# Optimization experiments

Measured on AMD Instinct MI355X. Metric: run time of the kernel, lower is better.

The kernel has to match this reference:

```python
import jax, jax.numpy as jnp
import numpy as np

N, E, G = 50000, 1600000, 500
H, F, NG, L, OUT = 128, 128, 50, 6, 1
LOG2 = float(np.log(2.0))

def ssp(x):
    return jax.nn.softplus(x) - LOG2

def setup_inputs() -> dict:
    key = jax.random.key(0)
    ks = jax.random.split(key, 16)
    inp = {
        'z': jax.random.randint(ks[0], (N,), 0, 100),
        'pos': jax.random.normal(ks[1], (N, 3), jnp.float32) * 5.0,
        'batch': jnp.sort(jax.random.randint(ks[2], (N,), 0, G)),
        'edge_index': jax.random.randint(ks[3], (2, E), 0, N),
        # parameters
        'emb': jax.random.normal(ks[4], (100, H), jnp.float32) * 0.1,
        'dist_W': jax.random.normal(ks[5], (1, NG), jnp.float32) * 0.1,
        'dist_b': jnp.zeros((NG,), jnp.float32),
        'Wn': jax.random.normal(ks[6], (L, H, F), jnp.float32) * (1.0 / np.sqrt(H)),
        'We': jax.random.normal(ks[7], (L, NG, F), jnp.float32) * (1.0 / np.sqrt(NG)),
        'be': jnp.zeros((L, F), jnp.float32),
        'Wo': jax.random.normal(ks[8], (L, F, H), jnp.float32) * (1.0 / np.sqrt(F)),
        'bo': jnp.zeros((L, H), jnp.float32),
        'W1': jax.random.normal(ks[9], (H, H // 2), jnp.float32) * (1.0 / np.sqrt(H)),
        'b1': jnp.zeros((H // 2,), jnp.float32),
        'W2': jax.random.normal(ks[10], (H // 2, OUT), jnp.float32) * (1.0 / np.sqrt(H // 2)),
        'b2': jnp.zeros((OUT,), jnp.float32),
    }
    return inp

def reference(z, pos, batch, edge_index, emb, dist_W, dist_b, Wn, We, be, Wo, bo, W1, b1, W2, b2):
    row, col = edge_index[0], edge_index[1]
    # edge distances -> Linear(1, num_gaussians)
    dist = jnp.linalg.norm(pos[row] - pos[col], axis=-1)            # [E]
    e = dist[:, None] * dist_W[0][None, :] + dist_b                 # [E, NG]
    v = emb[z]                                                      # [N, H]
    # edge-conditioned message passing x num_layers
    for i in range(Wn.shape[0]):
        h = v @ Wn[i]                                               # [N, F]
        msg = h[col] * (e @ We[i] + be[i])                          # [E, F]
        agg = jax.ops.segment_sum(msg, row, num_segments=v.shape[0])
        v = ssp(agg @ Wo[i] + bo[i])                                # [N, H]
    # readout
    u = ssp(v @ W1 + b1) @ W2 + b2                                  # [N, OUT]
    return jax.ops.segment_sum(u, batch, num_segments=G)            # [G, OUT]
```

## Files before the change

kernel.cpp:

```cpp
#include <hip/hip_runtime.h>
#include <math.h>

#define HDIM 128
#define NGAUSS 50
#define NLAYER 6
#define TSTR 136
#define DINV (1.0f/512.0f)
#define NXCD 8
#define NSTRIPE 512

typedef unsigned short ushortT;
typedef __attribute__((ext_vector_type(8))) short bf16x8;
typedef __attribute__((ext_vector_type(4))) float f32x4;

static __device__ __forceinline__ float bf2f(unsigned short u){
  union { unsigned int i; float f; } x; x.i = ((unsigned int)u) << 16; return x.f;
}
static __device__ __forceinline__ float bitsf(unsigned int i){
  union { unsigned int i; float f; } x; x.i = i; return x.f;
}
static __device__ __forceinline__ unsigned short f2bf(float f){
  union { float f; unsigned int i; } x; x.f = f;
  unsigned int i = x.i;
  unsigned int r = (i + 0x7FFFu + ((i >> 16) & 1u)) >> 16;
  return (unsigned short)r;
}
static __device__ __forceinline__ float ssp(float x){
  return fmaxf(x, 0.0f) + __logf(1.0f + __expf(-fabsf(x))) - 0.69314718055994530942f;
}
static __device__ __forceinline__ f32x4 mfma4r(const bf16x8* a, const bf16x8* b){
  f32x4 d = {0.f, 0.f, 0.f, 0.f};
  d = __builtin_amdgcn_mfma_f32_16x16x32_bf16(a[0], b[0], d, 0, 0, 0);
  d = __builtin_amdgcn_mfma_f32_16x16x32_bf16(a[1], b[1], d, 0, 0, 0);
  d = __builtin_amdgcn_mfma_f32_16x16x32_bf16(a[2], b[2], d, 0, 0, 0);
  d = __builtin_amdgcn_mfma_f32_16x16x32_bf16(a[3], b[3], d, 0, 0, 0);
  return d;
}


__global__ __launch_bounds__(256)
void k_hist(const int* __restrict__ erow, int* __restrict__ hist,
            int E, int NB, int shift, int estripe){
  __shared__ int lh[512];
  int tid = threadIdx.x, w = blockIdx.x;
  for (int i = tid; i < NB; i += 256) lh[i] = 0;
  __syncthreads();
  int beg = w * estripe;
  int end = beg + estripe; if (end > E) end = E;
  for (int e = beg + tid; e < end; e += 256)
    atomicAdd(&lh[erow[e] >> shift], 1);
  __syncthreads();
  for (int i = tid; i < NB; i += 256) hist[w * 512 + i] = lh[i];
}

__global__ __launch_bounds__(256)
void k_colscan(int* __restrict__ hist, int* __restrict__ colTotal, int NB){
  __shared__ int sA[512], sB[512];
  int b = blockIdx.x, tid = threadIdx.x;
  sA[tid]       = hist[tid * 512 + b];
  sA[tid + 256] = hist[(tid + 256) * 512 + b];
  __syncthreads();
  int* pa = sA; int* pb = sB;
  for (int off = 1; off < 512; off <<= 1){
    for (int i = tid; i < 512; i += 256)
      pb[i] = pa[i] + (i >= off ? pa[i - off] : 0);
    __syncthreads();
    int* t = pa; pa = pb; pb = t;
  }
  int e0 = (tid == 0) ? 0 : pa[tid - 1];
  int e1 = pa[tid + 255];
  hist[tid * 512 + b]       = e0;
  hist[(tid + 256) * 512 + b] = e1;
  if (tid == 0) colTotal[b] = pa[511];
}

__global__ __launch_bounds__(256)
void k_bscan(const int* __restrict__ colTotal, int* __restrict__ bucketBase, int NB){
  __shared__ int sA[512], sB[512];
  int tid = threadIdx.x;
  for (int i = tid; i < 512; i += 256) sA[i] = (i < NB) ? colTotal[i] : 0;
  __syncthreads();
  int* pa = sA; int* pb = sB;
  for (int off = 1; off < 512; off <<= 1){
    for (int i = tid; i < 512; i += 256)
      pb[i] = pa[i] + (i >= off ? pa[i - off] : 0);
    __syncthreads();
    int* t = pa; pa = pb; pb = t;
  }
  for (int i = tid; i < NB; i += 256)
    bucketBase[i] = (i == 0) ? 0 : pa[i - 1];
  if (tid == 0) bucketBase[NB] = pa[NB - 1];
}

__global__ __launch_bounds__(256)
void k_scatter(const int* __restrict__ erow, const int* __restrict__ ecol,
               const float* __restrict__ pos, const int* __restrict__ hist,
               const int* __restrict__ bucketBase, uint2* __restrict__ stg,
               int E, int NB, int shift, int estripe){
  __shared__ int cur[512];
  int tid = threadIdx.x, w = blockIdx.x;
  for (int b = tid; b < NB; b += 256)
    cur[b] = bucketBase[b] + hist[w * 512 + b];
  __syncthreads();
  int beg = w * estripe;
  int end = beg + estripe; if (end > E) end = E;
  int mask = (1 << shift) - 1;
  for (int e = beg + tid; e < end; e += 256){
    int r = erow[e], c = ecol[e];
    float dx = pos[r*3+0] - pos[c*3+0];
    float dy = pos[r*3+1] - pos[c*3+1];
    float dz = pos[r*3+2] - pos[c*3+2];
    float d = sqrtf(dx*dx + dy*dy + dz*dz);
    int du = (int)(d * 512.0f + 0.5f);
    if (du > 65535) du = 65535;
    int p = atomicAdd(&cur[r >> shift], 1);
    uint2 t;
    t.x = ((unsigned int)c << 16) | (unsigned int)du;
    t.y = (unsigned int)(r & mask);
    stg[p] = t;
  }
}

__global__ __launch_bounds__(256)
void k_place(const uint2* __restrict__ stg, const int* __restrict__ bucketBase,
             int* __restrict__ offsets, unsigned int* __restrict__ csr,
             int N, int NB, int shift, int E){
  __shared__ int rc[1024];
  __shared__ int sA[1024], sB[1024];
  int b = blockIdx.x, tid = threadIdx.x;
  int R = 1 << shift;
  int r0 = b << shift;
  int s = bucketBase[b], e2 = bucketBase[b + 1];
  for (int i = tid; i < R; i += 256) rc[i] = 0;
  __syncthreads();
  for (int j = s + tid; j < e2; j += 256)
    atomicAdd(&rc[stg[j].y], 1);
  __syncthreads();
  for (int i = tid; i < R; i += 256) sA[i] = rc[i];
  __syncthreads();
  int* pa = sA; int* pb = sB;
  for (int off = 1; off < R; off <<= 1){
    for (int i = tid; i < R; i += 256)
      pb[i] = pa[i] + (i >= off ? pa[i - off] : 0);
    __syncthreads();
    int* t = pa; pa = pb; pb = t;
  }
  for (int i = tid; i < R; i += 256){
    int excl = (i == 0) ? 0 : pa[i - 1];
    rc[i] = excl;
    int r = r0 + i;
    if (r < N) offsets[r] = s + excl;
  }
  if (b == NB - 1 && tid == 0) offsets[N] = E;
  __syncthreads();
  for (int j = s + tid; j < e2; j += 256){
    uint2 t = stg[j];
    int slot = s + atomicAdd(&rc[t.y], 1);
    csr[slot] = t.x;
  }
}

__global__ void k_setup(const int* __restrict__ z, const float* __restrict__ emb,
                        ushortT* __restrict__ vhi,
                        const float* __restrict__ Wn, ushortT* __restrict__ WnT,
                        const float* __restrict__ Wo, ushortT* __restrict__ WoT,
                        const float* __restrict__ dW, const float* __restrict__ db,
                        const float* __restrict__ We, const float* __restrict__ be,
                        float* __restrict__ a, float* __restrict__ c,
                        const int* __restrict__ batch, int* __restrict__ groupOff,
                        const float* __restrict__ W1, ushortT* __restrict__ W1T,
                        int N, int G, int B1, int B2, int B4, int B5, int B7){
  int b = blockIdx.x;
  int tid = threadIdx.x;
  if (b < B1){
    int idx = b * 256 + tid;
    if (idx < N * HDIM){
      int n = idx >> 7, f = idx & 127;
      vhi[idx] = f2bf(emb[z[n] * HDIM + f]);
    }
    return;
  }
  b -= B1;
  if (b < B2){
    int idx = b * 256 + tid;
    if (idx < NLAYER * HDIM * HDIM){
      int mat = idx >> 14, rem = idx & 16383;
      int n = rem >> 7, k = rem & 127;
      WnT[idx] = f2bf(Wn[(mat << 14) + k * HDIM + n]);
    }
    return;
  }
  b -= B2;
  if (b < B2){
    int idx = b * 256 + tid;
    if (idx < NLAYER * HDIM * HDIM){
      int mat = idx >> 14, rem = idx & 16383;
      int n = rem >> 7, k = rem & 127;
      WoT[idx] = f2bf(Wo[(mat << 14) + k * HDIM + n]);
    }
    return;
  }
  b -= B2;
  if (b < B4){
    int idx = b * 256 + tid;
    if (idx < NLAYER * HDIM){
      int l = idx >> 7, f = idx & 127;
      float av = 0.f, cv = 0.f;
      for (int g = 0; g < NGAUSS; ++g){
        float we = We[(l * NGAUSS + g) * HDIM + f];
        av += dW[g] * we;
        cv += db[g] * we;
      }
      a[idx] = av;
      c[idx] = cv + be[idx];
    }
    return;
  }
  b -= B4;
  if (b < B5){
    int i = b * 256 + tid;
    if (i >= N) return;
    int bb = batch[i];
    if (i == 0){
      for (int g = 0; g <= bb; ++g) groupOff[g] = 0;
    } else {
      int pb = batch[i - 1];
      for (int g = pb + 1; g <= bb; ++g) groupOff[g] = i;
    }
    if (i == N - 1){
      for (int g = bb + 1; g <= G; ++g) groupOff[g] = N;
    }
    return;
  }
  b -= B5;
  if (b < B7){
    int idx = b * 256 + tid;
    if (idx < 64 * HDIM){
      int ncol = idx >> 7, k = idx & 127;
      W1T[idx] = f2bf(W1[k * 64 + ncol]);
    }
  }
}

__global__ __launch_bounds__(128, 2)
void k_gemm0(const ushortT* __restrict__ X, const ushortT* __restrict__ WT,
             ushortT* __restrict__ outHi, int N){
  int tid = threadIdx.x;
  int wave = tid >> 6, lane = tid & 63;
  int m = lane & 15, quad = lane >> 4;
  int ntiles = (N + 15) >> 4;
  int t0 = (blockIdx.x * 2 + wave) * 2;
  if (t0 >= ntiles) return;

  bf16x8 av[2][4];
  #pragma unroll
  for (int rt = 0; rt < 2; ++rt){
    int row = (t0 + rt) * 16 + m; if (row >= N) row = N - 1;
    #pragma unroll
    for (int kk = 0; kk < 4; ++kk)
      av[rt][kk] = *(const bf16x8*)(X + ((size_t)row << 7) + kk*32 + quad*8);
  }
  #pragma unroll
  for (int ct = 0; ct < 8; ++ct){
    int ncol = ct * 16 + m;
    const ushortT* bp = WT + ((size_t)ncol << 7) + quad*8;
    bf16x8 bb[4];
    #pragma unroll
    for (int kk = 0; kk < 4; ++kk) bb[kk] = *(const bf16x8*)(bp + kk*32);
    #pragma unroll
    for (int rt = 0; rt < 2; ++rt){
      f32x4 d = mfma4r(av[rt], bb);
      #pragma unroll
      for (int r = 0; r < 4; ++r){
        int orow = (t0 + rt) * 16 + quad*4 + r;
        if (orow < N) outHi[((size_t)orow << 7) + ncol] = f2bf(d[r]);
      }
    }
  }
}

#define AGG_PROC(P, DD) do { \
    unsigned int w_; float lo_, hi_; \
    w_ = (P).x; lo_ = bitsf(w_ << 16); hi_ = bitsf(w_ & 0xFFFF0000u); \
    s1[0] = fmaf(lo_, (DD), s1[0]); s0[0] += lo_; \
    s1[1] = fmaf(hi_, (DD), s1[1]); s0[1] += hi_; \
    w_ = (P).y; lo_ = bitsf(w_ << 16); hi_ = bitsf(w_ & 0xFFFF0000u); \
    s1[2] = fmaf(lo_, (DD), s1[2]); s0[2] += lo_; \
    s1[3] = fmaf(hi_, (DD), s1[3]); s0[3] += hi_; \
    w_ = (P).z; lo_ = bitsf(w_ << 16); hi_ = bitsf(w_ & 0xFFFF0000u); \
    s1[4] = fmaf(lo_, (DD), s1[4]); s0[4] += lo_; \
    s1[5] = fmaf(hi_, (DD), s1[5]); s0[5] += hi_; \
    w_ = (P).w; lo_ = bitsf(w_ << 16); hi_ = bitsf(w_ & 0xFFFF0000u); \
    s1[6] = fmaf(lo_, (DD), s1[6]); s0[6] += lo_; \
    s1[7] = fmaf(hi_, (DD), s1[7]); s0[7] += hi_; \
  } while(0)

#define GATH(Q) (*(const uint4*)(h + ((size_t)((Q) >> 16) << 7) + fl))

__global__ __launch_bounds__(256, 6)
void k_agg2(const ushortT* __restrict__ h, const int* __restrict__ offsets,
            const unsigned int* __restrict__ cd, const float* __restrict__ a,
            const float* __restrict__ c, ushortT* __restrict__ aggHi,
            int N, int segNodes){
  int xcd = blockIdx.x & (NXCD - 1);
  int idx = blockIdx.x >> 3;
  int node = xcd * segNodes + idx * 4 + (threadIdx.x >> 6);
  if (node >= N || node >= (xcd + 1) * segNodes) return;
  int lane = threadIdx.x & 63;
  int quarter = lane >> 4;
  int fl = (lane & 15) * 8;
  int s = offsets[node], e = offsets[node + 1];
  float s0[8] = {0.f,0.f,0.f,0.f,0.f,0.f,0.f,0.f};
  float s1[8] = {0.f,0.f,0.f,0.f,0.f,0.f,0.f,0.f};
  int efull = s + ((e - s) & ~7);
  int L = s;
  if (efull - s >= 16){
    unsigned int qA0 = cd[L + quarter],      qA1 = cd[L + 4 + quarter];
    uint4 pA0 = GATH(qA0), pA1 = GATH(qA1);
    unsigned int qB0 = cd[L + 8 + quarter],  qB1 = cd[L + 12 + quarter];
    uint4 pB0 = GATH(qB0), pB1 = GATH(qB1);
    float dA0 = (float)(qA0 & 0xFFFFu) * DINV, dA1 = (float)(qA1 & 0xFFFFu) * DINV;
    float dB0 = (float)(qB0 & 0xFFFFu) * DINV, dB1 = (float)(qB1 & 0xFFFFu) * DINV;
    L += 16;
    for (; L + 16 <= efull; L += 16){
      unsigned int nA0 = cd[L + quarter], nA1 = cd[L + 4 + quarter];
      AGG_PROC(pA0, dA0); AGG_PROC(pA1, dA1);
      pA0 = GATH(nA0); pA1 = GATH(nA1);
      dA0 = (float)(nA0 & 0xFFFFu) * DINV; dA1 = (float)(nA1 & 0xFFFFu) * DINV;
      unsigned int nB0 = cd[L + 8 + quarter], nB1 = cd[L + 12 + quarter];
      AGG_PROC(pB0, dB0); AGG_PROC(pB1, dB1);
      pB0 = GATH(nB0); pB1 = GATH(nB1);
      dB0 = (float)(nB0 & 0xFFFFu) * DINV; dB1 = (float)(nB1 & 0xFFFFu) * DINV;
    }
    AGG_PROC(pA0, dA0); AGG_PROC(pA1, dA1);
    AGG_PROC(pB0, dB0); AGG_PROC(pB1, dB1);
  }
  for (; L + 8 <= efull; L += 8){
    unsigned int q0 = cd[L + quarter], q1 = cd[L + 4 + quarter];
    uint4 p0 = GATH(q0), p1 = GATH(q1);
    float d0 = (float)(q0 & 0xFFFFu) * DINV, d1 = (float)(q1 & 0xFFFFu) * DINV;
    AGG_PROC(p0, d0); AGG_PROC(p1, d1);
  }
  for (int j = efull; j < e; j += 4){
    int myj = j + quarter;
    if (myj < e){
      unsigned int q = cd[myj];
      uint4 p = GATH(q);
      float dd = (float)(q & 0xFFFFu) * DINV;
      AGG_PROC(p, dd);
    }
  }
  float4 av0 = *(const float4*)(a + fl);
  float4 av1 = *(const float4*)(a + fl + 4);
  float4 cv0 = *(const float4*)(c + fl);
  float4 cv1 = *(const float4*)(c + fl + 4);
  float r[8];
  r[0] = av0.x * s1[0] + cv0.x * s0[0];
  r[1] = av0.y * s1[1] + cv0.y * s0[1];
  r[2] = av0.z * s1[2] + cv0.z * s0[2];
  r[3] = av0.w * s1[3] + cv0.w * s0[3];
  r[4] = av1.x * s1[4] + cv1.x * s0[4];
  r[5] = av1.y * s1[5] + cv1.y * s0[5];
  r[6] = av1.z * s1[6] + cv1.z * s0[6];
  r[7] = av1.w * s1[7] + cv1.w * s0[7];
  #pragma unroll
  for (int k = 0; k < 8; ++k){
    r[k] += __shfl_down(r[k], 32, 64);
    r[k] += __shfl_down(r[k], 16, 64);
  }
  if (quarter == 0){
    uint4 st;
    st.x = (unsigned int)f2bf(r[0]) | ((unsigned int)f2bf(r[1]) << 16);
    st.y = (unsigned int)f2bf(r[2]) | ((unsigned int)f2bf(r[3]) << 16);
    st.z = (unsigned int)f2bf(r[4]) | ((unsigned int)f2bf(r[5]) << 16);
    st.w = (unsigned int)f2bf(r[6]) | ((unsigned int)f2bf(r[7]) << 16);
    *(uint4*)(aggHi + ((size_t)node << 7) + fl) = st;
  }
}

__global__ __launch_bounds__(256, 2)
void k_fpair(const ushortT* __restrict__ agg, const ushortT* __restrict__ WoT,
             const float* __restrict__ bo, const ushortT* __restrict__ WnT,
             ushortT* __restrict__ outH, int N, int segTiles){
  __shared__ ushortT vt[4][16 * TSTR];
  int tid = threadIdx.x;
  int wave = tid >> 6, lane = tid & 63;
  int m = lane & 15, quad = lane >> 4;
  int ntiles = (N + 15) >> 4;
  int xcd = blockIdx.x & (NXCD - 1);
  int idx = blockIdx.x >> 3;
  int tIdx = idx * 4 + wave;
  if (tIdx >= segTiles) return;
  int t0 = xcd * segTiles + tIdx;
  if (t0 >= ntiles) return;
  ushortT* vw = vt[wave];

  bf16x8 av[4];
  int row = t0 * 16 + m; if (row >= N) row = N - 1;
  #pragma unroll
  for (int kk = 0; kk < 4; ++kk)
    av[kk] = *(const bf16x8*)(agg + ((size_t)row << 7) + kk*32 + quad*8);
  #pragma unroll
  for (int ct = 0; ct < 8; ++ct){
    int ncol = ct * 16 + m;
    const ushortT* bp = WoT + ((size_t)ncol << 7) + quad*8;
    bf16x8 bb[4];
    #pragma unroll
    for (int kk = 0; kk < 4; ++kk) bb[kk] = *(const bf16x8*)(bp + kk*32);
    float bbias = bo[ncol];
    f32x4 d = mfma4r(av, bb);
    #pragma unroll
    for (int r = 0; r < 4; ++r)
      vw[(quad*4 + r) * TSTR + ncol] = f2bf(ssp(d[r] + bbias));
  }
  bf16x8 a2[4];
  #pragma unroll
  for (int kk = 0; kk < 4; ++kk)
    a2[kk] = *(const bf16x8*)(&vw[m * TSTR + kk*32 + quad*8]);
  #pragma unroll
  for (int ct = 0; ct < 8; ++ct){
    int ncol = ct * 16 + m;
    const ushortT* bp = WnT + ((size_t)ncol << 7) + quad*8;
    bf16x8 bb[4];
    #pragma unroll
    for (int kk = 0; kk < 4; ++kk) bb[kk] = *(const bf16x8*)(bp + kk*32);
    f32x4 d = mfma4r(a2, bb);
    #pragma unroll
    for (int r = 0; r < 4; ++r){
      int orow = t0 * 16 + quad*4 + r;
      if (orow < N) outH[((size_t)orow << 7) + ncol] = f2bf(d[r]);
    }
  }
}

__global__ __launch_bounds__(256, 2)
void k_gfinal(const ushortT* __restrict__ agg, const ushortT* __restrict__ WoT,
              const float* __restrict__ bo, const ushortT* __restrict__ W1T,
              const float* __restrict__ b1, const float* __restrict__ W2,
              const float* __restrict__ b2, float* __restrict__ u,
              int N, int segTiles){
  __shared__ ushortT vt[4][16 * TSTR];
  int tid = threadIdx.x;
  int wave = tid >> 6, lane = tid & 63;
  int m = lane & 15, quad = lane >> 4;
  int ntiles = (N + 15) >> 4;
  int xcd = blockIdx.x & (NXCD - 1);
  int idx = blockIdx.x >> 3;
  int tIdx = idx * 4 + wave;
  if (tIdx >= segTiles) return;
  int t0 = xcd * segTiles + tIdx;
  if (t0 >= ntiles) return;
  ushortT* vw = vt[wave];

  bf16x8 av[4];
  int row = t0 * 16 + m; if (row >= N) row = N - 1;
  #pragma unroll
  for (int kk = 0; kk < 4; ++kk)
    av[kk] = *(const bf16x8*)(agg + ((size_t)row << 7) + kk*32 + quad*8);
  #pragma unroll
  for (int ct = 0; ct < 8; ++ct){
    int ncol = ct * 16 + m;
    const ushortT* bp = WoT + ((size_t)ncol << 7) + quad*8;
    bf16x8 bb[4];
    #pragma unroll
    for (int kk = 0; kk < 4; ++kk) bb[kk] = *(const bf16x8*)(bp + kk*32);
    float bbias = bo[ncol];
    f32x4 d = mfma4r(av, bb);
    #pragma unroll
    for (int r = 0; r < 4; ++r)
      vw[(quad*4 + r) * TSTR + ncol] = f2bf(ssp(d[r] + bbias));
  }
  bf16x8 a2[4];
  #pragma unroll
  for (int kk = 0; kk < 4; ++kk)
    a2[kk] = *(const bf16x8*)(&vw[m * TSTR + kk*32 + quad*8]);
  float acc[4] = {0.f,0.f,0.f,0.f};
  #pragma unroll
  for (int ct = 0; ct < 4; ++ct){
    int ncol = ct * 16 + m;
    const ushortT* bp = W1T + ((size_t)ncol << 7) + quad*8;
    bf16x8 bb[4];
    #pragma unroll
    for (int kk = 0; kk < 4; ++kk) bb[kk] = *(const bf16x8*)(bp + kk*32);
    float bb1 = b1[ncol];
    float w2  = W2[ncol];
    f32x4 d = mfma4r(a2, bb);
    #pragma unroll
    for (int r = 0; r < 4; ++r)
      acc[r] += ssp(d[r] + bb1) * w2;
  }
  float bb2 = b2[0];
  #pragma unroll
  for (int r = 0; r < 4; ++r){
    float v = acc[r];
    v += __shfl_xor(v, 1, 64);
    v += __shfl_xor(v, 2, 64);
    v += __shfl_xor(v, 4, 64);
    v += __shfl_xor(v, 8, 64);
    if (m == 0){
      int orow = t0 * 16 + quad*4 + r;
      if (orow < N) u[orow] = v + bb2;
    }
  }
}

__global__ void k_gsum(const float* __restrict__ u, const int* __restrict__ groupOff,
                       float* __restrict__ out, int G){
  int g = blockIdx.x * 4 + (threadIdx.x >> 6);
  if (g >= G) return;
  int lane = threadIdx.x & 63;
  int s = groupOff[g], e = groupOff[g + 1];
  float acc = 0.f;
  for (int j = s + lane; j < e; j += 64) acc += u[j];
  #pragma unroll
  for (int off = 32; off > 0; off >>= 1)
    acc += __shfl_down(acc, off, 64);
  if (lane == 0) out[g] = acc;
}

extern "C" void kernel_launch(void* const* d_in, const int* in_sizes, int n_in,
                              void* d_out, int out_size, void* d_ws, size_t ws_size,
                              hipStream_t stream){
  const int N = in_sizes[0];
  const int E = in_sizes[3] / 2;
  const int G = out_size;

  const int*   z     = (const int*)d_in[0];
  const float* pos   = (const float*)d_in[1];
  const int*   batch = (const int*)d_in[2];
  const int*   eidx  = (const int*)d_in[3];
  const int*   erow  = eidx;
  const int*   ecol  = eidx + E;
  const float* emb   = (const float*)d_in[4];
  const float* dW    = (const float*)d_in[5];
  const float* db    = (const float*)d_in[6];
  const float* Wn    = (const float*)d_in[7];
  const float* We    = (const float*)d_in[8];
  const float* be    = (const float*)d_in[9];
  const float* Wo    = (const float*)d_in[10];
  const float* bo    = (const float*)d_in[11];
  const float* W1    = (const float*)d_in[12];
  const float* b1    = (const float*)d_in[13];
  const float* W2    = (const float*)d_in[14];
  const float* b2    = (const float*)d_in[15];

  char* ws = (char*)d_ws;
  size_t off = 0;
  auto alloc = [&](size_t bytes) -> char* {
    char* p = ws + off;
    off = (off + bytes + 255) & ~(size_t)255;
    return p;
  };
  size_t hbytes = (size_t)N * HDIM * 2;
  size_t stgbytes = (size_t)E * 8;
  int*          offsets  = (int*)         alloc((size_t)(N + 1) * 4);
  unsigned int* csr      = (unsigned int*)alloc((size_t)E * 4);
  ushortT*      h0       = (ushortT*)     alloc(hbytes);
  ushortT*      h1       = (ushortT*)     alloc(hbytes);
  ushortT*      vhi      = (ushortT*)     alloc(hbytes);
  ushortT*      agghi    = (ushortT*)     alloc(hbytes);
  ushortT*      stgbuf   = (ushortT*)     alloc(stgbytes);
  ushortT*      WnT      = (ushortT*)     alloc((size_t)NLAYER * HDIM * HDIM * 2);
  ushortT*      WoT      = (ushortT*)     alloc((size_t)NLAYER * HDIM * HDIM * 2);
  ushortT*      W1T      = (ushortT*)     alloc((size_t)64 * HDIM * 2);
  float*        a        = (float*)       alloc((size_t)NLAYER * HDIM * 4);
  float*        c        = (float*)       alloc((size_t)NLAYER * HDIM * 4);
  float*        u        = (float*)       alloc((size_t)N * 4);
  int*          groupOff = (int*)         alloc((size_t)(G + 1) * 4);

  int*   hist       = (int*)h1;
  int*   colTotal   = hist + NSTRIPE * 512;
  int*   bucketBase = colTotal + 512;
  uint2* stg        = (uint2*)stgbuf;

  int shift = 7;
  while ((((N - 1) >> shift) + 1) > 512) ++shift;
  int NB = ((N - 1) >> shift) + 1;
  int estripe = (E + NSTRIPE - 1) / NSTRIPE;

  int B1 = (N * HDIM + 255) / 256;
  int B2 = (NLAYER * HDIM * HDIM + 255) / 256;
  int B4 = (NLAYER * HDIM + 255) / 256;
  int B5 = (N + 255) / 256;
  int B7 = (64 * HDIM + 255) / 256;
  k_setup<<<B1 + 2*B2 + B4 + B5 + B7, 256, 0, stream>>>(
      z, emb, vhi, Wn, WnT, Wo, WoT,
      dW, db, We, be, a, c, batch, groupOff, W1, W1T,
      N, G, B1, B2, B4, B5, B7);

  k_hist   <<<NSTRIPE, 256, 0, stream>>>(erow, hist, E, NB, shift, estripe);
  k_colscan<<<NB,      256, 0, stream>>>(hist, colTotal, NB);
  k_bscan  <<<1,       256, 0, stream>>>(colTotal, bucketBase, NB);
  k_scatter<<<NSTRIPE, 256, 0, stream>>>(erow, ecol, pos, hist, bucketBase,
                                         stg, E, NB, shift, estripe);
  k_place  <<<NB,      256, 0, stream>>>(stg, bucketBase, offsets, csr, N, NB, shift, E);

  int ntiles = (N + 15) >> 4;
  int segTiles = (((ntiles + NXCD - 1) / NXCD) + 1) & ~1;
  int segNodes = segTiles * 16;
  int aggGrid  = NXCD * ((segNodes + 3) / 4);
  int gGrid    = NXCD * ((segTiles + 3) / 4);
  int nwj = (ntiles + 1) / 2;
  int pairGrid = (nwj + 1) / 2;
  k_gemm0<<<pairGrid, 128, 0, stream>>>(vhi, WnT, h0, N);

  for (int l = 0; l < NLAYER; ++l){
    size_t wo = (size_t)l * HDIM * HDIM;
    const ushortT* hin  = (l & 1) ? h1 : h0;
    ushortT*       hout = (l & 1) ? h0 : h1;
    k_agg2<<<aggGrid, 256, 0, stream>>>(hin, offsets, csr,
                                        a + l * HDIM, c + l * HDIM, agghi, N, segNodes);
    if (l < NLAYER - 1){
      size_t wn = (size_t)(l + 1) * HDIM * HDIM;
      k_fpair<<<gGrid, 256, 0, stream>>>(agghi, WoT + wo, bo + (size_t)l * HDIM,
                                         WnT + wn, hout, N, segTiles);
    } else {
      k_gfinal<<<gGrid, 256, 0, stream>>>(agghi, WoT + wo, bo + (size_t)l * HDIM,
                                          W1T, b1, W2, b2, u, N, segTiles);
    }
  }
  k_gsum<<<(G + 3) / 4, 256, 0, stream>>>(u, groupOff, (float*)d_out, G);
}
```

Baseline: 645.9 us.

## Fuse edge aggregation with per-tile node GEMMs into one kernel per layer

Merges the gather-aggregate kernel with the following Wo/Wn (or readout) GEMM kernel. Each 256-thread block now aggregates a 16-node tile into LDS, then splits the two 16x128x128 MFMA stages across its four waves by output columns, with block barriers between stages. This removes the bf16 agg buffer's global write and re-read and one launch per layer. The cost is that each wave now aggregates four nodes serially, which lowers per-node gather parallelism, and the barriers can expose imbalance in node degree.

After: 722.4 us. 1.12x slower.

```diff
diff --git a/kernel.cpp b/kernel.cpp
--- a/kernel.cpp
+++ b/kernel.cpp
@@ -297,57 +297,52 @@
 
 #define GATH(Q) (*(const uint4*)(h + ((size_t)((Q) >> 16) << 7) + fl))
 
-__global__ __launch_bounds__(256, 6)
-void k_agg2(const ushortT* __restrict__ h, const int* __restrict__ offsets,
-            const unsigned int* __restrict__ cd, const float* __restrict__ a,
-            const float* __restrict__ c, ushortT* __restrict__ aggHi,
-            int N, int segNodes){
-  int xcd = blockIdx.x & (NXCD - 1);
-  int idx = blockIdx.x >> 3;
-  int node = xcd * segNodes + idx * 4 + (threadIdx.x >> 6);
-  if (node >= N || node >= (xcd + 1) * segNodes) return;
-  int lane = threadIdx.x & 63;
-  int quarter = lane >> 4;
-  int fl = (lane & 15) * 8;
-  int s = offsets[node], e = offsets[node + 1];
+static __device__ __forceinline__ void agg_row(
+    const ushortT* __restrict__ h, const int* __restrict__ offsets,
+    const unsigned int* __restrict__ cd, const float* __restrict__ a,
+    const float* __restrict__ c, ushortT* __restrict__ tile,
+    int node, int row, int N, int quarter, int fl){
   float s0[8] = {0.f,0.f,0.f,0.f,0.f,0.f,0.f,0.f};
   float s1[8] = {0.f,0.f,0.f,0.f,0.f,0.f,0.f,0.f};
-  int efull = s + ((e - s) & ~7);
-  int L = s;
-  if (efull - s >= 16){
-    unsigned int qA0 = cd[L + quarter],      qA1 = cd[L + 4 + quarter];
-    uint4 pA0 = GATH(qA0), pA1 = GATH(qA1);
-    unsigned int qB0 = cd[L + 8 + quarter],  qB1 = cd[L + 12 + quarter];
-    uint4 pB0 = GATH(qB0), pB1 = GATH(qB1);
-    float dA0 = (float)(qA0 & 0xFFFFu) * DINV, dA1 = (float)(qA1 & 0xFFFFu) * DINV;
-    float dB0 = (float)(qB0 & 0xFFFFu) * DINV, dB1 = (float)(qB1 & 0xFFFFu) * DINV;
-    L += 16;
-    for (; L + 16 <= efull; L += 16){
-      unsigned int nA0 = cd[L + quarter], nA1 = cd[L + 4 + quarter];
+  if (node < N){
+    int s = offsets[node], e = offsets[node + 1];
+    int efull = s + ((e - s) & ~7);
+    int L = s;
+    if (efull - s >= 16){
+      unsigned int qA0 = cd[L + quarter],      qA1 = cd[L + 4 + quarter];
+      uint4 pA0 = GATH(qA0), pA1 = GATH(qA1);
+      unsigned int qB0 = cd[L + 8 + quarter],  qB1 = cd[L + 12 + quarter];
+      uint4 pB0 = GATH(qB0), pB1 = GATH(qB1);
+      float dA0 = (float)(qA0 & 0xFFFFu) * DINV, dA1 = (float)(qA1 & 0xFFFFu) * DINV;
+      float dB0 = (float)(qB0 & 0xFFFFu) * DINV, dB1 = (float)(qB1 & 0xFFFFu) * DINV;
+      L += 16;
+      for (; L + 16 <= efull; L += 16){
+        unsigned int nA0 = cd[L + quarter], nA1 = cd[L + 4 + quarter];
+        AGG_PROC(pA0, dA0); AGG_PROC(pA1, dA1);
+        pA0 = GATH(nA0); pA1 = GATH(nA1);
+        dA0 = (float)(nA0 & 0xFFFFu) * DINV; dA1 = (float)(nA1 & 0xFFFFu) * DINV;
+        unsigned int nB0 = cd[L + 8 + quarter], nB1 = cd[L + 12 + quarter];
+        AGG_PROC(pB0, dB0); AGG_PROC(pB1, dB1);
+        pB0 = GATH(nB0); pB1 = GATH(nB1);
+        dB0 = (float)(nB0 & 0xFFFFu) * DINV; dB1 = (float)(nB1 & 0xFFFFu) * DINV;
+      }
       AGG_PROC(pA0, dA0); AGG_PROC(pA1, dA1);
-      pA0 = GATH(nA0); pA1 = GATH(nA1);
-      dA0 = (float)(nA0 & 0xFFFFu) * DINV; dA1 = (float)(nA1 & 0xFFFFu) * DINV;
-      unsigned int nB0 = cd[L + 8 + quarter], nB1 = cd[L + 12 + quarter];
       AGG_PROC(pB0, dB0); AGG_PROC(pB1, dB1);
-      pB0 = GATH(nB0); pB1 = GATH(nB1);
-      dB0 = (float)(nB0 & 0xFFFFu) * DINV; dB1 = (float)(nB1 & 0xFFFFu) * DINV;
-    }
-    AGG_PROC(pA0, dA0); AGG_PROC(pA1, dA1);
-    AGG_PROC(pB0, dB0); AGG_PROC(pB1, dB1);
-  }
-  for (; L + 8 <= efull; L += 8){
-    unsigned int q0 = cd[L + quarter], q1 = cd[L + 4 + quarter];
-    uint4 p0 = GATH(q0), p1 = GATH(q1);
-    float d0 = (float)(q0 & 0xFFFFu) * DINV, d1 = (float)(q1 & 0xFFFFu) * DINV;
-    AGG_PROC(p0, d0); AGG_PROC(p1, d1);
-  }
-  for (int j = efull; j < e; j += 4){
-    int myj = j + quarter;
-    if (myj < e){
-      unsigned int q = cd[myj];
-      uint4 p = GATH(q);
-      float dd = (float)(q & 0xFFFFu) * DINV;
-      AGG_PROC(p, dd);
+    }
+    for (; L + 8 <= efull; L += 8){
+      unsigned int q0 = cd[L + quarter], q1 = cd[L + 4 + quarter];
+      uint4 p0 = GATH(q0), p1 = GATH(q1);
+      float d0 = (float)(q0 & 0xFFFFu) * DINV, d1 = (float)(q1 & 0xFFFFu) * DINV;
+      AGG_PROC(p0, d0); AGG_PROC(p1, d1);
+    }
+    for (int j = efull; j < e; j += 4){
+      int myj = j + quarter;
+      if (myj < e){
+        unsigned int q = cd[myj];
+        uint4 p = GATH(q);
+        float dd = (float)(q & 0xFFFFu) * DINV;
+        AGG_PROC(p, dd);
+      }
     }
   }
   float4 av0 = *(const float4*)(a + fl);
@@ -374,35 +369,42 @@
     st.y = (unsigned int)f2bf(r[2]) | ((unsigned int)f2bf(r[3]) << 16);
     st.z = (unsigned int)f2bf(r[4]) | ((unsigned int)f2bf(r[5]) << 16);
     st.w = (unsigned int)f2bf(r[6]) | ((unsigned int)f2bf(r[7]) << 16);
-    *(uint4*)(aggHi + ((size_t)node << 7) + fl) = st;
-  }
-}
-
-__global__ __launch_bounds__(256, 2)
-void k_fpair(const ushortT* __restrict__ agg, const ushortT* __restrict__ WoT,
-             const float* __restrict__ bo, const ushortT* __restrict__ WnT,
-             ushortT* __restrict__ outH, int N, int segTiles){
-  __shared__ ushortT vt[4][16 * TSTR];
-  int tid = threadIdx.x;
-  int wave = tid >> 6, lane = tid & 63;
-  int m = lane & 15, quad = lane >> 4;
-  int ntiles = (N + 15) >> 4;
+    *(uint4*)(tile + row * TSTR + fl) = st;
+  }
+}
+
+__global__ __launch_bounds__(256, 6)
+void k_aggf(const ushortT* __restrict__ h, const int* __restrict__ offsets,
+            const unsigned int* __restrict__ cd, const float* __restrict__ a,
+            const float* __restrict__ c, const ushortT* __restrict__ WoT,
+            const float* __restrict__ bo, const ushortT* __restrict__ WnT,
+            ushortT* __restrict__ outH, int N, int segTiles){
+  __shared__ ushortT t1[16 * TSTR];
+  __shared__ ushortT t2[16 * TSTR];
   int xcd = blockIdx.x & (NXCD - 1);
   int idx = blockIdx.x >> 3;
-  int tIdx = idx * 4 + wave;
-  if (tIdx >= segTiles) return;
-  int t0 = xcd * segTiles + tIdx;
+  if (idx >= segTiles) return;
+  int t0 = xcd * segTiles + idx;
+  int ntiles = (N + 15) >> 4;
   if (t0 >= ntiles) return;
-  ushortT* vw = vt[wave];
+  int tid = threadIdx.x, wave = tid >> 6, lane = tid & 63;
+  int quarter = lane >> 4;
+  int fl = (lane & 15) * 8;
+  int m = lane & 15, quad = quarter;
+
+  for (int i = 0; i < 4; ++i){
+    int row = wave * 4 + i;
+    agg_row(h, offsets, cd, a, c, t1, t0 * 16 + row, row, N, quarter, fl);
+  }
+  __syncthreads();
 
   bf16x8 av[4];
-  int row = t0 * 16 + m; if (row >= N) row = N - 1;
   #pragma unroll
   for (int kk = 0; kk < 4; ++kk)
-    av[kk] = *(const bf16x8*)(agg + ((size_t)row << 7) + kk*32 + quad*8);
-  #pragma unroll
-  for (int ct = 0; ct < 8; ++ct){
-    int ncol = ct * 16 + m;
+    av[kk] = *(const bf16x8*)(&t1[m * TSTR + kk*32 + quad*8]);
+  #pragma unroll
+  for (int cti = 0; cti < 2; ++cti){
+    int ncol = (wave * 2 + cti) * 16 + m;
     const ushortT* bp = WoT + ((size_t)ncol << 7) + quad*8;
     bf16x8 bb[4];
     #pragma unroll
@@ -411,15 +413,17 @@
     f32x4 d = mfma4r(av, bb);
     #pragma unroll
     for (int r = 0; r < 4; ++r)
-      vw[(quad*4 + r) * TSTR + ncol] = f2bf(ssp(d[r] + bbias));
-  }
+      t2[(quad*4 + r) * TSTR + ncol] = f2bf(ssp(d[r] + bbias));
+  }
+  __syncthreads();
+
   bf16x8 a2[4];
   #pragma unroll
   for (int kk = 0; kk < 4; ++kk)
-    a2[kk] = *(const bf16x8*)(&vw[m * TSTR + kk*32 + quad*8]);
-  #pragma unroll
-  for (int ct = 0; ct < 8; ++ct){
-    int ncol = ct * 16 + m;
+    a2[kk] = *(const bf16x8*)(&t2[m * TSTR + kk*32 + quad*8]);
+  #pragma unroll
+  for (int cti = 0; cti < 2; ++cti){
+    int ncol = (wave * 2 + cti) * 16 + m;
     const ushortT* bp = WnT + ((size_t)ncol << 7) + quad*8;
     bf16x8 bb[4];
     #pragma unroll
@@ -433,33 +437,41 @@
   }
 }
 
-__global__ __launch_bounds__(256, 2)
-void k_gfinal(const ushortT* __restrict__ agg, const ushortT* __restrict__ WoT,
-              const float* __restrict__ bo, const ushortT* __restrict__ W1T,
-              const float* __restrict__ b1, const float* __restrict__ W2,
-              const float* __restrict__ b2, float* __restrict__ u,
-              int N, int segTiles){
-  __shared__ ushortT vt[4][16 * TSTR];
-  int tid = threadIdx.x;
-  int wave = tid >> 6, lane = tid & 63;
-  int m = lane & 15, quad = lane >> 4;
-  int ntiles = (N + 15) >> 4;
+__global__ __launch_bounds__(256, 6)
+void k_aggl(const ushortT* __restrict__ h, const int* __restrict__ offsets,
+            const unsigned int* __restrict__ cd, const float* __restrict__ a,
+            const float* __restrict__ c, const ushortT* __restrict__ WoT,
+            const float* __restrict__ bo, const ushortT* __restrict__ W1T,
+            const float* __restrict__ b1, const float* __restrict__ W2,
+            const float* __restrict__ b2, float* __restrict__ u,
+            int N, int segTiles){
+  __shared__ ushortT t1[16 * TSTR];
+  __shared__ ushortT t2[16 * TSTR];
+  __shared__ float part[4][16];
   int xcd = blockIdx.x & (NXCD - 1);
   int idx = blockIdx.x >> 3;
-  int tIdx = idx * 4 + wave;
-  if (tIdx >= segTiles) return;
-  int t0 = xcd * segTiles + tIdx;
+  if (idx >= segTiles) return;
+  int t0 = xcd * segTiles + idx;
+  int ntiles = (N + 15) >> 4;
   if (t0 >= ntiles) return;
-  ushortT* vw = vt[wave];
+  int tid = threadIdx.x, wave = tid >> 6, lane = tid & 63;
+  int quarter = lane >> 4;
+  int fl = (lane & 15) * 8;
+  int m = lane & 15, quad = quarter;
+
+  for (int i = 0; i < 4; ++i){
+    int row = wave * 4 + i;
+    agg_row(h, offsets, cd, a, c, t1, t0 * 16 + row, row, N, quarter, fl);
+  }
+  __syncthreads();
 
   bf16x8 av[4];
-  int row = t0 * 16 + m; if (row >= N) row = N - 1;
   #pragma unroll
   for (int kk = 0; kk < 4; ++kk)
-    av[kk] = *(const bf16x8*)(agg + ((size_t)row << 7) + kk*32 + quad*8);
-  #pragma unroll
-  for (int ct = 0; ct < 8; ++ct){
-    int ncol = ct * 16 + m;
+    av[kk] = *(const bf16x8*)(&t1[m * TSTR + kk*32 + quad*8]);
+  #pragma unroll
+  for (int cti = 0; cti < 2; ++cti){
+    int ncol = (wave * 2 + cti) * 16 + m;
     const ushortT* bp = WoT + ((size_t)ncol << 7) + quad*8;
     bf16x8 bb[4];
     #pragma unroll
@@ -468,39 +480,41 @@
     f32x4 d = mfma4r(av, bb);
     #pragma unroll
     for (int r = 0; r < 4; ++r)
-      vw[(quad*4 + r) * TSTR + ncol] = f2bf(ssp(d[r] + bbias));
-  }
+      t2[(quad*4 + r) * TSTR + ncol] = f2bf(ssp(d[r] + bbias));
+  }
+  __syncthreads();
+
   bf16x8 a2[4];
   #pragma unroll
   for (int kk = 0; kk < 4; ++kk)
-    a2[kk] = *(const bf16x8*)(&vw[m * TSTR + kk*32 + quad*8]);
-  float acc[4] = {0.f,0.f,0.f,0.f};
-  #pragma unroll
-  for (int ct = 0; ct < 4; ++ct){
-    int ncol = ct * 16 + m;
-    const ushortT* bp = W1T + ((size_t)ncol << 7) + quad*8;
-    bf16x8 bb[4];
-    #pragma unroll
-    for (int kk = 0; kk < 4; ++kk) bb[kk] = *(const bf16x8*)(bp + kk*32);
-    float bb1 = b1[ncol];
-    float w2  = W2[ncol];
-    f32x4 d = mfma4r(a2, bb);
-    #pragma unroll
-    for (int r = 0; r < 4; ++r)
-      acc[r] += ssp(d[r] + bb1) * w2;
-  }
-  float bb2 = b2[0];
+    a2[kk] = *(const bf16x8*)(&t2[m * TSTR + kk*32 + quad*8]);
+  int ncol = wave * 16 + m;
+  const ushortT* bp = W1T + ((size_t)ncol << 7) + quad*8;
+  bf16x8 bb[4];
+  #pragma unroll
+  for (int kk = 0; kk < 4; ++kk) bb[kk] = *(const bf16x8*)(bp + kk*32);
+  float bb1 = b1[ncol];
+  float w2  = W2[ncol];
+  f32x4 d = mfma4r(a2, bb);
+  float acc[4];
   #pragma unroll
   for (int r = 0; r < 4; ++r){
-    float v = acc[r];
+    float v = ssp(d[r] + bb1) * w2;
     v += __shfl_xor(v, 1, 64);
     v += __shfl_xor(v, 2, 64);
     v += __shfl_xor(v, 4, 64);
     v += __shfl_xor(v, 8, 64);
-    if (m == 0){
-      int orow = t0 * 16 + quad*4 + r;
-      if (orow < N) u[orow] = v + bb2;
-    }
+    acc[r] = v;
+  }
+  if (m == 0){
+    #pragma unroll
+    for (int r = 0; r < 4; ++r) part[wave][quad*4 + r] = acc[r];
+  }
+  __syncthreads();
+  if (tid < 16){
+    float v = part[0][tid] + part[1][tid] + part[2][tid] + part[3][tid] + b2[0];
+    int orow = t0 * 16 + tid;
+    if (orow < N) u[orow] = v;
   }
 }
 
@@ -558,7 +572,6 @@
   ushortT*      h0       = (ushortT*)     alloc(hbytes);
   ushortT*      h1       = (ushortT*)     alloc(hbytes);
   ushortT*      vhi      = (ushortT*)     alloc(hbytes);
-  ushortT*      agghi    = (ushortT*)     alloc(hbytes);
   ushortT*      stgbuf   = (ushortT*)     alloc(stgbytes);
   ushortT*      WnT      = (ushortT*)     alloc((size_t)NLAYER * HDIM * HDIM * 2);
   ushortT*      WoT      = (ushortT*)     alloc((size_t)NLAYER * HDIM * HDIM * 2);
@@ -597,9 +610,7 @@
 
   int ntiles = (N + 15) >> 4;
   int segTiles = (((ntiles + NXCD - 1) / NXCD) + 1) & ~1;
-  int segNodes = segTiles * 16;
-  int aggGrid  = NXCD * ((segNodes + 3) / 4);
-  int gGrid    = NXCD * ((segTiles + 3) / 4);
+  int fusedGrid = NXCD * segTiles;
   int nwj = (ntiles + 1) / 2;
   int pairGrid = (nwj + 1) / 2;
   k_gemm0<<<pairGrid, 128, 0, stream>>>(vhi, WnT, h0, N);
@@ -608,15 +619,17 @@
     size_t wo = (size_t)l * HDIM * HDIM;
     const ushortT* hin  = (l & 1) ? h1 : h0;
     ushortT*       hout = (l & 1) ? h0 : h1;
-    k_agg2<<<aggGrid, 256, 0, stream>>>(hin, offsets, csr,
-                                        a + l * HDIM, c + l * HDIM, agghi, N, segNodes);
     if (l < NLAYER - 1){
       size_t wn = (size_t)(l + 1) * HDIM * HDIM;
-      k_fpair<<<gGrid, 256, 0, stream>>>(agghi, WoT + wo, bo + (size_t)l * HDIM,
-                                         WnT + wn, hout, N, segTiles);
+      k_aggf<<<fusedGrid, 256, 0, stream>>>(hin, offsets, csr,
+                                            a + l * HDIM, c + l * HDIM,
+                                            WoT + wo, bo + (size_t)l * HDIM,
+                                            WnT + wn, hout, N, segTiles);
     } else {
-      k_gfinal<<<gGrid, 256, 0, stream>>>(agghi, WoT + wo, bo + (size_t)l * HDIM,
-                                          W1T, b1, W2, b2, u, N, segTiles);
+      k_aggl<<<fusedGrid, 256, 0, stream>>>(hin, offsets, csr,
+                                            a + l * HDIM, c + l * HDIM,
+                                            WoT + wo, bo + (size_t)l * HDIM,
+                                            W1T, b1, W2, b2, u, N, segTiles);
     }
   }
   k_gsum<<<(G + 3) / 4, 256, 0, stream>>>(u, groupOff, (float*)d_out, G);
```
